# Kernel optimization log

Measured on AMD Instinct MI355X. Metric: run time of the kernel, lower is better.

Reference implementation:

```python
import jax, jax.numpy as jnp
import numpy as np

N_NODES = 50000
N_EDGES = 800000
EMB = 96
HID = 2 * EMB


def setup_inputs() -> dict:
    key = jax.random.key(0)
    ks = jax.random.split(key, 8)
    h = jax.random.normal(ks[0], (N_NODES, EMB), dtype=jnp.float32)
    edge_attr = jax.random.normal(ks[1], (N_EDGES, EMB), dtype=jnp.float32)
    src = jax.random.randint(ks[2], (N_EDGES,), 0, N_NODES, dtype=jnp.int32)
    dst = jax.random.randint(ks[3], (N_EDGES,), 0, N_NODES, dtype=jnp.int32)
    W1 = jax.random.normal(ks[4], (EMB, HID), dtype=jnp.float32) * (1.0 / np.sqrt(EMB))
    b1 = jnp.zeros((HID,), dtype=jnp.float32)
    W2 = jax.random.normal(ks[5], (HID, EMB), dtype=jnp.float32) * (1.0 / np.sqrt(HID))
    b2 = jnp.zeros((EMB,), dtype=jnp.float32)
    eps = jnp.zeros((1,), dtype=jnp.float32)
    return {"h": h, "edge_attr": edge_attr, "src": src, "dst": dst,
            "W1": W1, "b1": b1, "W2": W2, "b2": b2, "eps": eps}


def reference(h, edge_attr, src, dst, W1, b1, W2, b2, eps):
    # message: m_e = h[src_e] + edge_attr_e   -> [E, EMB]
    m = h[src] + edge_attr
    # reduce: sum messages per destination node -> [N, EMB]
    aggr = jax.ops.segment_sum(m, dst, num_segments=N_NODES)
    # 2-layer MLP: Linear(EMB, 2*EMB) -> ReLU -> Linear(2*EMB, EMB)
    hidden = jax.nn.relu(aggr @ W1 + b1)
    mlp_out = hidden @ W2 + b2
    # GIN update: (1 + eps) * h + MLP(aggr)
    out = (1.0 + eps[0]) * h + mlp_out
    return out
```

## Files before the change

kernel.cpp:

```cpp
#include <hip/hip_runtime.h>

#define N_NODES 50000
#define N_EDGES 800000
#define EMB 96
#define HID 192
#define BN 64
#define BJ 64
#define KT 32

__global__ __launch_bounds__(256) void hist_kernel(
    const int* __restrict__ dst, int* __restrict__ counts)
{
    int e = blockIdx.x * 256 + threadIdx.x;
    if (e < N_EDGES) atomicAdd(&counts[dst[e]], 1);
}

__global__ __launch_bounds__(1024) void scan_kernel(
    const int* __restrict__ counts, int* __restrict__ offsets)
{
    __shared__ int wave_sums[16];
    int t = threadIdx.x;
    int lane = t & 63, wave = t >> 6;
    int running = 0;
    for (int base = 0; base < N_NODES; base += 1024) {
        int v = (base + t < N_NODES) ? counts[base + t] : 0;
        int x = v;
        #pragma unroll
        for (int d = 1; d < 64; d <<= 1) {
            int y = __shfl_up(x, d);
            if (lane >= d) x += y;
        }
        if (lane == 63) wave_sums[wave] = x;
        __syncthreads();
        if (t < 16) {
            int s = wave_sums[t];
            #pragma unroll
            for (int d = 1; d < 16; d <<= 1) {
                int y = __shfl_up(s, d);
                if (t >= d) s += y;
            }
            wave_sums[t] = s;
        }
        __syncthreads();
        int woff = wave ? wave_sums[wave - 1] : 0;
        if (base + t < N_NODES) offsets[base + t] = running + woff + x - v;
        int total = wave_sums[15];
        __syncthreads();
        running += total;
    }
    if (t == 0) offsets[N_NODES] = running;
}

__global__ __launch_bounds__(256) void fill_kernel(
    const int* __restrict__ src, const int* __restrict__ dst,
    const int* __restrict__ offsets, int* __restrict__ cursor,
    int2* __restrict__ pairs)
{
    int e = blockIdx.x * 256 + threadIdx.x;
    if (e < N_EDGES) {
        int d = dst[e];
        int pos = offsets[d] + atomicAdd(&cursor[d], 1);
        pairs[pos] = make_int2(e, src[e]);
    }
}

__global__ __launch_bounds__(192) void gather_kernel(
    const float4* __restrict__ h4, const float4* __restrict__ ea4,
    const int* __restrict__ offsets, const int2* __restrict__ pairs,
    float4* __restrict__ aggr4)
{
    int n = blockIdx.x * 8 + threadIdx.x / 24;
    int c = threadIdx.x % 24;
    if (n >= N_NODES) return;
    int beg = offsets[n], end = offsets[n + 1];
    float4 acc = make_float4(0.f, 0.f, 0.f, 0.f);
    int i = beg;
    int2 p = (i < end) ? pairs[i] : make_int2(0, 0);
    while (i < end) {
        int2 cur = p;
        ++i;
        if (i < end) p = pairs[i];
        float4 a = ea4[(size_t)cur.x * 24 + c];
        float4 b = h4[(size_t)cur.y * 24 + c];
        acc.x += a.x + b.x;
        acc.y += a.y + b.y;
        acc.z += a.z + b.z;
        acc.w += a.w + b.w;
    }
    aggr4[(size_t)n * 24 + c] = acc;
}

__global__ __launch_bounds__(256) void mlp1_kernel(
    const float* __restrict__ aggr, const float* __restrict__ W1,
    const float* __restrict__ b1, float* __restrict__ hidden)
{
    __shared__ float sA[BN][EMB + 1];
    __shared__ float sW[EMB][BJ];
    int n0 = blockIdx.x * BN;
    int j0 = blockIdx.y * BJ;
    int t = threadIdx.x;

    for (int i = t; i < BN * (EMB / 4); i += 256) {
        int row = i / (EMB / 4);
        int c   = i % (EMB / 4);
        float4 v = make_float4(0.f, 0.f, 0.f, 0.f);
        if (n0 + row < N_NODES)
            v = ((const float4*)aggr)[(size_t)(n0 + row) * (EMB / 4) + c];
        sA[row][c * 4 + 0] = v.x; sA[row][c * 4 + 1] = v.y;
        sA[row][c * 4 + 2] = v.z; sA[row][c * 4 + 3] = v.w;
    }
    for (int i = t; i < EMB * (BJ / 4); i += 256) {
        int k = i / (BJ / 4);
        int c = i % (BJ / 4);
        float4 v = *(const float4*)(W1 + (size_t)k * HID + j0 + c * 4);
        *(float4*)&sW[k][c * 4] = v;
    }
    __syncthreads();

    int tx = t % 16, ty = t / 16;
    float acc[4][4];
    float4 bv = *(const float4*)(b1 + j0 + tx * 4);
    for (int i = 0; i < 4; ++i) {
        acc[i][0] = bv.x; acc[i][1] = bv.y; acc[i][2] = bv.z; acc[i][3] = bv.w;
    }
    for (int k = 0; k < EMB; ++k) {
        float a0 = sA[ty * 4 + 0][k];
        float a1 = sA[ty * 4 + 1][k];
        float a2 = sA[ty * 4 + 2][k];
        float a3 = sA[ty * 4 + 3][k];
        float4 w = *(float4*)&sW[k][tx * 4];
        acc[0][0] += a0 * w.x; acc[0][1] += a0 * w.y; acc[0][2] += a0 * w.z; acc[0][3] += a0 * w.w;
        acc[1][0] += a1 * w.x; acc[1][1] += a1 * w.y; acc[1][2] += a1 * w.z; acc[1][3] += a1 * w.w;
        acc[2][0] += a2 * w.x; acc[2][1] += a2 * w.y; acc[2][2] += a2 * w.z; acc[2][3] += a2 * w.w;
        acc[3][0] += a3 * w.x; acc[3][1] += a3 * w.y; acc[3][2] += a3 * w.z; acc[3][3] += a3 * w.w;
    }
    for (int i = 0; i < 4; ++i) {
        int n = n0 + ty * 4 + i;
        if (n < N_NODES) {
            float4 o;
            o.x = fmaxf(acc[i][0], 0.f);
            o.y = fmaxf(acc[i][1], 0.f);
            o.z = fmaxf(acc[i][2], 0.f);
            o.w = fmaxf(acc[i][3], 0.f);
            ((float4*)hidden)[(size_t)n * (HID / 4) + (j0 / 4) + tx] = o;
        }
    }
}

__global__ __launch_bounds__(384) void mlp2_kernel(
    const float* __restrict__ hidden, const float* __restrict__ W2,
    const float* __restrict__ b2, const float* __restrict__ h,
    const float* __restrict__ eps, float* __restrict__ out)
{
    __shared__ float sH[BN][KT + 1];
    __shared__ float sW[KT][EMB];
    int n0 = blockIdx.x * BN;
    int t = threadIdx.x;
    int tx = t % 24, ty = t / 24;

    float acc[4][4];
    float4 bv = *(const float4*)(b2 + tx * 4);
    for (int i = 0; i < 4; ++i) {
        acc[i][0] = bv.x; acc[i][1] = bv.y; acc[i][2] = bv.z; acc[i][3] = bv.w;
    }

    for (int kt = 0; kt < HID; kt += KT) {
        __syncthreads();
        for (int i = t; i < BN * (KT / 4); i += 384) {
            int row = i / (KT / 4);
            int c   = i % (KT / 4);
            float4 v = make_float4(0.f, 0.f, 0.f, 0.f);
            if (n0 + row < N_NODES)
                v = ((const float4*)hidden)[(size_t)(n0 + row) * (HID / 4) + kt / 4 + c];
            sH[row][c * 4 + 0] = v.x; sH[row][c * 4 + 1] = v.y;
            sH[row][c * 4 + 2] = v.z; sH[row][c * 4 + 3] = v.w;
        }
        for (int i = t; i < KT * (EMB / 4); i += 384) {
            int kr = i / (EMB / 4);
            int c  = i % (EMB / 4);
            *(float4*)&sW[kr][c * 4] = *(const float4*)(W2 + (size_t)(kt + kr) * EMB + c * 4);
        }
        __syncthreads();
        for (int k = 0; k < KT; ++k) {
            float a0 = sH[ty * 4 + 0][k];
            float a1 = sH[ty * 4 + 1][k];
            float a2 = sH[ty * 4 + 2][k];
            float a3 = sH[ty * 4 + 3][k];
            float4 w = *(float4*)&sW[k][tx * 4];
            acc[0][0] += a0 * w.x; acc[0][1] += a0 * w.y; acc[0][2] += a0 * w.z; acc[0][3] += a0 * w.w;
            acc[1][0] += a1 * w.x; acc[1][1] += a1 * w.y; acc[1][2] += a1 * w.z; acc[1][3] += a1 * w.w;
            acc[2][0] += a2 * w.x; acc[2][1] += a2 * w.y; acc[2][2] += a2 * w.z; acc[2][3] += a2 * w.w;
            acc[3][0] += a3 * w.x; acc[3][1] += a3 * w.y; acc[3][2] += a3 * w.z; acc[3][3] += a3 * w.w;
        }
    }

    float scale = 1.f + eps[0];
    for (int i = 0; i < 4; ++i) {
        int n = n0 + ty * 4 + i;
        if (n < N_NODES) {
            float4 hv = ((const float4*)h)[(size_t)n * (EMB / 4) + tx];
            float4 o;
            o.x = acc[i][0] + scale * hv.x;
            o.y = acc[i][1] + scale * hv.y;
            o.z = acc[i][2] + scale * hv.z;
            o.w = acc[i][3] + scale * hv.w;
            ((float4*)out)[(size_t)n * (EMB / 4) + tx] = o;
        }
    }
}

extern "C" void kernel_launch(void* const* d_in, const int* in_sizes, int n_in,
                              void* d_out, int out_size, void* d_ws, size_t ws_size,
                              hipStream_t stream) {
    const float* h         = (const float*)d_in[0];
    const float* edge_attr = (const float*)d_in[1];
    const int*   src       = (const int*)d_in[2];
    const int*   dst       = (const int*)d_in[3];
    const float* W1        = (const float*)d_in[4];
    const float* b1        = (const float*)d_in[5];
    const float* W2        = (const float*)d_in[6];
    const float* b2        = (const float*)d_in[7];
    const float* eps       = (const float*)d_in[8];
    float* out    = (float*)d_out;

    float* aggr    = (float*)d_ws;
    float* hidden  = aggr + (size_t)N_NODES * EMB;
    int2*  pairs   = (int2*)(hidden + (size_t)N_NODES * HID);
    int*   offsets = (int*)(pairs + N_EDGES);
    int*   counts  = offsets + N_NODES + 1;
    int*   cursor  = counts + N_NODES;

    hipMemsetAsync(counts, 0, (size_t)2 * N_NODES * sizeof(int), stream);

    hist_kernel<<<(N_EDGES + 255) / 256, 256, 0, stream>>>(dst, counts);
    scan_kernel<<<1, 1024, 0, stream>>>(counts, offsets);
    fill_kernel<<<(N_EDGES + 255) / 256, 256, 0, stream>>>(src, dst, offsets, cursor, pairs);
    gather_kernel<<<(N_NODES + 7) / 8, 192, 0, stream>>>(
        (const float4*)h, (const float4*)edge_attr, offsets, pairs, (float4*)aggr);

    dim3 g1((N_NODES + BN - 1) / BN, HID / BJ);
    mlp1_kernel<<<g1, 256, 0, stream>>>(aggr, W1, b1, hidden);

    int g2 = (N_NODES + BN - 1) / BN;
    mlp2_kernel<<<g2, 384, 0, stream>>>(hidden, W2, b2, h, eps, out);
}
```

Before: 668.2 us.

## Run MLP layers on bf16 MFMA with bf16 intermediates and pre-transposed weights

```diff
diff --git a/kernel.cpp b/kernel.cpp
--- a/kernel.cpp
+++ b/kernel.cpp
@@ -4,9 +4,16 @@
 #define N_EDGES 800000
 #define EMB 96
 #define HID 192
-#define BN 64
-#define BJ 64
-#define KT 32
+
+typedef __attribute__((ext_vector_type(8))) short short8;
+typedef __attribute__((ext_vector_type(4))) float f32x4;
+typedef __attribute__((ext_vector_type(4))) unsigned short ushort4v;
+
+static __device__ __forceinline__ unsigned short f2bf(float f) {
+    union { float f; unsigned int u; } v; v.f = f;
+    unsigned int u = v.u;
+    return (unsigned short)((u + 0x7FFFu + ((u >> 16) & 1u)) >> 16);
+}
 
 __global__ __launch_bounds__(256) void hist_kernel(
     const int* __restrict__ dst, int* __restrict__ counts)
@@ -64,10 +71,25 @@
     }
 }
 
+__global__ __launch_bounds__(256) void conv_kernel(
+    const float* __restrict__ W1, const float* __restrict__ W2,
+    unsigned short* __restrict__ W1t, unsigned short* __restrict__ W2t)
+{
+    int i = blockIdx.x * 256 + threadIdx.x;
+    if (i < EMB * HID) {
+        int n = i / EMB, k = i % EMB;
+        W1t[i] = f2bf(W1[(size_t)k * HID + n]);
+    } else if (i < 2 * EMB * HID) {
+        int j = i - EMB * HID;
+        int n = j / HID, k = j % HID;
+        W2t[j] = f2bf(W2[(size_t)k * EMB + n]);
+    }
+}
+
 __global__ __launch_bounds__(192) void gather_kernel(
     const float4* __restrict__ h4, const float4* __restrict__ ea4,
     const int* __restrict__ offsets, const int2* __restrict__ pairs,
-    float4* __restrict__ aggr4)
+    unsigned short* __restrict__ aggr_bf)
 {
     int n = blockIdx.x * 8 + threadIdx.x / 24;
     int c = threadIdx.x % 24;
@@ -87,124 +109,96 @@
         acc.z += a.z + b.z;
         acc.w += a.w + b.w;
     }
-    aggr4[(size_t)n * 24 + c] = acc;
-}
-
-__global__ __launch_bounds__(256) void mlp1_kernel(
-    const float* __restrict__ aggr, const float* __restrict__ W1,
-    const float* __restrict__ b1, float* __restrict__ hidden)
-{
-    __shared__ float sA[BN][EMB + 1];
-    __shared__ float sW[EMB][BJ];
-    int n0 = blockIdx.x * BN;
-    int j0 = blockIdx.y * BJ;
+    ushort4v o;
+    o.x = f2bf(acc.x); o.y = f2bf(acc.y); o.z = f2bf(acc.z); o.w = f2bf(acc.w);
+    *(ushort4v*)(aggr_bf + (size_t)n * EMB + c * 4) = o;
+}
+
+__global__ __launch_bounds__(256) void mlp1_mfma(
+    const unsigned short* __restrict__ aggr_bf,
+    const unsigned short* __restrict__ W1t,
+    const float* __restrict__ b1,
+    unsigned short* __restrict__ hidden_bf)
+{
+    __shared__ unsigned short sW[HID * 104];
     int t = threadIdx.x;
-
-    for (int i = t; i < BN * (EMB / 4); i += 256) {
-        int row = i / (EMB / 4);
-        int c   = i % (EMB / 4);
-        float4 v = make_float4(0.f, 0.f, 0.f, 0.f);
-        if (n0 + row < N_NODES)
-            v = ((const float4*)aggr)[(size_t)(n0 + row) * (EMB / 4) + c];
-        sA[row][c * 4 + 0] = v.x; sA[row][c * 4 + 1] = v.y;
-        sA[row][c * 4 + 2] = v.z; sA[row][c * 4 + 3] = v.w;
-    }
-    for (int i = t; i < EMB * (BJ / 4); i += 256) {
-        int k = i / (BJ / 4);
-        int c = i % (BJ / 4);
-        float4 v = *(const float4*)(W1 + (size_t)k * HID + j0 + c * 4);
-        *(float4*)&sW[k][c * 4] = v;
+    const unsigned int* srcp = (const unsigned int*)W1t;
+    for (int i = t; i < HID * (EMB / 2); i += 256) {
+        int n = i / (EMB / 2), c = i % (EMB / 2);
+        *(unsigned int*)&sW[n * 104 + c * 2] = srcp[(size_t)n * (EMB / 2) + c];
     }
     __syncthreads();
-
-    int tx = t % 16, ty = t / 16;
-    float acc[4][4];
-    float4 bv = *(const float4*)(b1 + j0 + tx * 4);
-    for (int i = 0; i < 4; ++i) {
-        acc[i][0] = bv.x; acc[i][1] = bv.y; acc[i][2] = bv.z; acc[i][3] = bv.w;
-    }
-    for (int k = 0; k < EMB; ++k) {
-        float a0 = sA[ty * 4 + 0][k];
-        float a1 = sA[ty * 4 + 1][k];
-        float a2 = sA[ty * 4 + 2][k];
-        float a3 = sA[ty * 4 + 3][k];
-        float4 w = *(float4*)&sW[k][tx * 4];
-        acc[0][0] += a0 * w.x; acc[0][1] += a0 * w.y; acc[0][2] += a0 * w.z; acc[0][3] += a0 * w.w;
-        acc[1][0] += a1 * w.x; acc[1][1] += a1 * w.y; acc[1][2] += a1 * w.z; acc[1][3] += a1 * w.w;
-        acc[2][0] += a2 * w.x; acc[2][1] += a2 * w.y; acc[2][2] += a2 * w.z; acc[2][3] += a2 * w.w;
-        acc[3][0] += a3 * w.x; acc[3][1] += a3 * w.y; acc[3][2] += a3 * w.z; acc[3][3] += a3 * w.w;
-    }
-    for (int i = 0; i < 4; ++i) {
-        int n = n0 + ty * 4 + i;
-        if (n < N_NODES) {
-            float4 o;
-            o.x = fmaxf(acc[i][0], 0.f);
-            o.y = fmaxf(acc[i][1], 0.f);
-            o.z = fmaxf(acc[i][2], 0.f);
-            o.w = fmaxf(acc[i][3], 0.f);
-            ((float4*)hidden)[(size_t)n * (HID / 4) + (j0 / 4) + tx] = o;
-        }
-    }
-}
-
-__global__ __launch_bounds__(384) void mlp2_kernel(
-    const float* __restrict__ hidden, const float* __restrict__ W2,
-    const float* __restrict__ b2, const float* __restrict__ h,
-    const float* __restrict__ eps, float* __restrict__ out)
-{
-    __shared__ float sH[BN][KT + 1];
-    __shared__ float sW[KT][EMB];
-    int n0 = blockIdx.x * BN;
+    int wave = t >> 6, lane = t & 63;
+    int m0 = (blockIdx.x * 4 + wave) * 16;
+    if (m0 >= N_NODES) return;
+    int quad = lane >> 4, col = lane & 15;
+    f32x4 acc[12];
+    #pragma unroll
+    for (int c = 0; c < 12; ++c) acc[c] = (f32x4){0.f, 0.f, 0.f, 0.f};
+    int m = m0 + col;
+    #pragma unroll
+    for (int ks = 0; ks < 3; ++ks) {
+        short8 af = *(const short8*)(aggr_bf + (size_t)m * EMB + ks * 32 + quad * 8);
+        #pragma unroll
+        for (int c = 0; c < 12; ++c) {
+            short8 bf = *(const short8*)(sW + (c * 16 + col) * 104 + ks * 32 + quad * 8);
+            acc[c] = __builtin_amdgcn_mfma_f32_16x16x32_bf16(af, bf, acc[c], 0, 0, 0);
+        }
+    }
+    #pragma unroll
+    for (int c = 0; c < 12; ++c) {
+        float bias = b1[c * 16 + col];
+        #pragma unroll
+        for (int r = 0; r < 4; ++r) {
+            int row = m0 + quad * 4 + r;
+            float v = fmaxf(acc[c][r] + bias, 0.f);
+            hidden_bf[(size_t)row * HID + c * 16 + col] = f2bf(v);
+        }
+    }
+}
+
+__global__ __launch_bounds__(256) void mlp2_mfma(
+    const unsigned short* __restrict__ hidden_bf,
+    const unsigned short* __restrict__ W2t,
+    const float* __restrict__ b2,
+    const float* __restrict__ h,
+    const float* __restrict__ eps,
+    float* __restrict__ out)
+{
+    __shared__ unsigned short sW[EMB * 200];
     int t = threadIdx.x;
-    int tx = t % 24, ty = t / 24;
-
-    float acc[4][4];
-    float4 bv = *(const float4*)(b2 + tx * 4);
-    for (int i = 0; i < 4; ++i) {
-        acc[i][0] = bv.x; acc[i][1] = bv.y; acc[i][2] = bv.z; acc[i][3] = bv.w;
-    }
-
-    for (int kt = 0; kt < HID; kt += KT) {
-        __syncthreads();
-        for (int i = t; i < BN * (KT / 4); i += 384) {
-            int row = i / (KT / 4);
-            int c   = i % (KT / 4);
-            float4 v = make_float4(0.f, 0.f, 0.f, 0.f);
-            if (n0 + row < N_NODES)
-                v = ((const float4*)hidden)[(size_t)(n0 + row) * (HID / 4) + kt / 4 + c];
-            sH[row][c * 4 + 0] = v.x; sH[row][c * 4 + 1] = v.y;
-            sH[row][c * 4 + 2] = v.z; sH[row][c * 4 + 3] = v.w;
-        }
-        for (int i = t; i < KT * (EMB / 4); i += 384) {
-            int kr = i / (EMB / 4);
-            int c  = i % (EMB / 4);
-            *(float4*)&sW[kr][c * 4] = *(const float4*)(W2 + (size_t)(kt + kr) * EMB + c * 4);
-        }
-        __syncthreads();
-        for (int k = 0; k < KT; ++k) {
-            float a0 = sH[ty * 4 + 0][k];
-            float a1 = sH[ty * 4 + 1][k];
-            float a2 = sH[ty * 4 + 2][k];
-            float a3 = sH[ty * 4 + 3][k];
-            float4 w = *(float4*)&sW[k][tx * 4];
-            acc[0][0] += a0 * w.x; acc[0][1] += a0 * w.y; acc[0][2] += a0 * w.z; acc[0][3] += a0 * w.w;
-            acc[1][0] += a1 * w.x; acc[1][1] += a1 * w.y; acc[1][2] += a1 * w.z; acc[1][3] += a1 * w.w;
-            acc[2][0] += a2 * w.x; acc[2][1] += a2 * w.y; acc[2][2] += a2 * w.z; acc[2][3] += a2 * w.w;
-            acc[3][0] += a3 * w.x; acc[3][1] += a3 * w.y; acc[3][2] += a3 * w.z; acc[3][3] += a3 * w.w;
-        }
-    }
-
-    float scale = 1.f + eps[0];
-    for (int i = 0; i < 4; ++i) {
-        int n = n0 + ty * 4 + i;
-        if (n < N_NODES) {
-            float4 hv = ((const float4*)h)[(size_t)n * (EMB / 4) + tx];
-            float4 o;
-            o.x = acc[i][0] + scale * hv.x;
-            o.y = acc[i][1] + scale * hv.y;
-            o.z = acc[i][2] + scale * hv.z;
-            o.w = acc[i][3] + scale * hv.w;
-            ((float4*)out)[(size_t)n * (EMB / 4) + tx] = o;
+    const unsigned int* srcp = (const unsigned int*)W2t;
+    for (int i = t; i < EMB * (HID / 2); i += 256) {
+        int n = i / (HID / 2), c = i % (HID / 2);
+        *(unsigned int*)&sW[n * 200 + c * 2] = srcp[(size_t)n * (HID / 2) + c];
+    }
+    __syncthreads();
+    int wave = t >> 6, lane = t & 63;
+    int m0 = (blockIdx.x * 4 + wave) * 16;
+    if (m0 >= N_NODES) return;
+    int quad = lane >> 4, col = lane & 15;
+    f32x4 acc[6];
+    #pragma unroll
+    for (int c = 0; c < 6; ++c) acc[c] = (f32x4){0.f, 0.f, 0.f, 0.f};
+    int m = m0 + col;
+    #pragma unroll
+    for (int ks = 0; ks < 6; ++ks) {
+        short8 af = *(const short8*)(hidden_bf + (size_t)m * HID + ks * 32 + quad * 8);
+        #pragma unroll
+        for (int c = 0; c < 6; ++c) {
+            short8 bf = *(const short8*)(sW + (c * 16 + col) * 200 + ks * 32 + quad * 8);
+            acc[c] = __builtin_amdgcn_mfma_f32_16x16x32_bf16(af, bf, acc[c], 0, 0, 0);
+        }
+    }
+    float s = 1.f + eps[0];
+    #pragma unroll
+    for (int c = 0; c < 6; ++c) {
+        float bias = b2[c * 16 + col];
+        #pragma unroll
+        for (int r = 0; r < 4; ++r) {
+            int row = m0 + quad * 4 + r;
+            size_t idx = (size_t)row * EMB + c * 16 + col;
+            out[idx] = acc[c][r] + bias + s * h[idx];
         }
     }
 }
@@ -221,26 +215,27 @@
     const float* W2        = (const float*)d_in[6];
     const float* b2        = (const float*)d_in[7];
     const float* eps       = (const float*)d_in[8];
-    float* out    = (float*)d_out;
-
-    float* aggr    = (float*)d_ws;
-    float* hidden  = aggr + (size_t)N_NODES * EMB;
-    int2*  pairs   = (int2*)(hidden + (size_t)N_NODES * HID);
-    int*   offsets = (int*)(pairs + N_EDGES);
-    int*   counts  = offsets + N_NODES + 1;
-    int*   cursor  = counts + N_NODES;
+    float* out = (float*)d_out;
+
+    unsigned char* wsp = (unsigned char*)d_ws;
+    unsigned short* aggr_bf   = (unsigned short*)wsp; wsp += (size_t)N_NODES * EMB * 2;
+    unsigned short* hidden_bf = (unsigned short*)wsp; wsp += (size_t)N_NODES * HID * 2;
+    unsigned short* W1t       = (unsigned short*)wsp; wsp += (size_t)EMB * HID * 2;
+    unsigned short* W2t       = (unsigned short*)wsp; wsp += (size_t)EMB * HID * 2;
+    int2* pairs   = (int2*)wsp; wsp += (size_t)N_EDGES * sizeof(int2);
+    int*  offsets = (int*)wsp;  wsp += (size_t)(N_NODES + 1) * sizeof(int);
+    int*  counts  = (int*)wsp;  wsp += (size_t)N_NODES * sizeof(int);
+    int*  cursor  = (int*)wsp;
 
     hipMemsetAsync(counts, 0, (size_t)2 * N_NODES * sizeof(int), stream);
 
     hist_kernel<<<(N_EDGES + 255) / 256, 256, 0, stream>>>(dst, counts);
     scan_kernel<<<1, 1024, 0, stream>>>(counts, offsets);
     fill_kernel<<<(N_EDGES + 255) / 256, 256, 0, stream>>>(src, dst, offsets, cursor, pairs);
+    conv_kernel<<<(2 * EMB * HID + 255) / 256, 256, 0, stream>>>(W1, W2, W1t, W2t);
     gather_kernel<<<(N_NODES + 7) / 8, 192, 0, stream>>>(
-        (const float4*)h, (const float4*)edge_attr, offsets, pairs, (float4*)aggr);
-
-    dim3 g1((N_NODES + BN - 1) / BN, HID / BJ);
-    mlp1_kernel<<<g1, 256, 0, stream>>>(aggr, W1, b1, hidden);
-
-    int g2 = (N_NODES + BN - 1) / BN;
-    mlp2_kernel<<<g2, 384, 0, stream>>>(hidden, W2, b2, h, eps, out);
-}
+        (const float4*)h, (const float4*)edge_attr, offsets, pairs, aggr_bf);
+
+    mlp1_mfma<<<(N_NODES / 16 + 3) / 4, 256, 0, stream>>>(aggr_bf, W1t, b1, hidden_bf);
+    mlp2_mfma<<<(N_NODES / 16 + 3) / 4, 256, 0, stream>>>(hidden_bf, W2t, b2, h, eps, out);
+}
```

Result: faster. 615.8 us (-7.8%).
